# Performance work log

Hardware: AMD Instinct MI355X
Metric: run time of the kernel (lower is better)

The kernel has to match this reference:

```python
import jax, jax.numpy as jnp
import numpy as np

NUM_INPUTS = 16
NUM_HIDDEN = 256
NUM_LAYERS = 4
B = 16384


def setup_inputs() -> dict:
    key = jax.random.key(0)
    ks = jax.random.split(key, 8)
    H, N, L = NUM_HIDDEN, NUM_INPUTS, NUM_LAYERS
    x0 = jax.random.normal(ks[0], (B, N), dtype=jnp.float32)
    # input layer: Linear(2 -> H)
    W_in = jax.random.normal(ks[1], (2, H), dtype=jnp.float32) * (1.0 / np.sqrt(2.0))
    b_in = jnp.zeros((H,), dtype=jnp.float32)
    # L-1 intermediate layers: Linear(2H -> H), stacked
    W_mid = jax.random.normal(ks[2], (L - 1, 2 * H, H), dtype=jnp.float32) * (1.0 / np.sqrt(2.0 * H))
    b_mid = jnp.zeros((L - 1, H), dtype=jnp.float32)
    # slater: Linear(H -> N) with xavier-normal weight, zero bias
    W_sl = jax.random.normal(ks[3], (H, N), dtype=jnp.float32) * np.sqrt(2.0 / (H + N))
    b_sl = jnp.zeros((N,), dtype=jnp.float32)
    width = jnp.full((1,), 0.1, dtype=jnp.float32)
    return {"x0": x0, "W_in": W_in, "b_in": b_in, "W_mid": W_mid,
            "b_mid": b_mid, "W_sl": W_sl, "b_sl": b_sl, "width": width}


def _forward(x0, W_in, b_in, W_mid, b_mid, W_sl, b_sl, width):
    N = x0.shape[1]
    # input equivariant layer: f = stack(h, mean(h)) -> [B, N, 2]
    g = jnp.broadcast_to(x0.mean(axis=1, keepdims=True), x0.shape)
    f = jnp.stack((x0, g), axis=2)                       # [B, N, 2]
    h = jnp.tanh(jnp.einsum('bnf,fh->bnh', f, W_in) + b_in)  # [B, N, H]
    # intermediate equivariant layers with residual
    for i in range(W_mid.shape[0]):
        gm = jnp.broadcast_to(h.mean(axis=1, keepdims=True), h.shape)
        fm = jnp.concatenate((h, gm), axis=2)            # [B, N, 2H]
        h = jnp.tanh(jnp.einsum('bnf,fh->bnh', fm, W_mid[i]) + b_mid[i]) + h
    # slog slater determinant
    slater = jnp.einsum('bnh,hm->bnm', h, W_sl) + b_sl   # [B, N, N]
    sign, logabsdet = jnp.linalg.slogdet(slater)
    log_factorial = jnp.log(jnp.arange(1, N + 1, dtype=jnp.float32)).sum()
    log_bcs = -width[0] * jnp.sum(x0 ** 2, axis=1)       # [B]
    return sign, logabsdet - 0.5 * log_factorial + log_bcs


def reference(x0, W_in, b_in, W_mid, b_mid, W_sl, b_sl, width):
    return _forward(x0, W_in, b_in, W_mid, b_mid, W_sl, b_sl, width)
```

## Files before the change

### kernel.cpp

```cpp
#include <hip/hip_runtime.h>

#define BTOT 16384
#define NI   16
#define HD   256
#define BB   4
#define NMID 3
#define ASH  264
#define SLS  20
#define HALF_LOGFACT 15.3359295387f

typedef short  bf16x8 __attribute__((ext_vector_type(8)));
typedef float  f32x4  __attribute__((ext_vector_type(4)));

__device__ __forceinline__ unsigned short f2bf(float f) {
    unsigned u = __builtin_bit_cast(unsigned, f);
    u += 0x7FFFu + ((u >> 16) & 1u);
    return (unsigned short)(u >> 16);
}
__device__ __forceinline__ unsigned cvt_pk_bf16(float lo, float hi) {
    unsigned d;
    asm("v_cvt_pk_bf16_f32 %0, %1, %2" : "=v"(d) : "v"(lo), "v"(hi));
    return d;
}
__device__ __forceinline__ float bflo(unsigned u) { return __builtin_bit_cast(float, u << 16); }
__device__ __forceinline__ float bfhi(unsigned u) { return __builtin_bit_cast(float, u & 0xFFFF0000u); }
__device__ __forceinline__ float bcast(float x, int lane) {
    return __builtin_bit_cast(float,
        __builtin_amdgcn_readlane(__builtin_bit_cast(int, x), lane));
}
__device__ __forceinline__ float tanh5(float x) {
    float z = __builtin_amdgcn_exp2f(x * 2.885390081777927f);
    return __builtin_fmaf(-2.0f, __builtin_amdgcn_rcpf(1.0f + z), 1.0f);
}
#define LGKM_BAR() do { asm volatile("s_waitcnt lgkmcnt(0)" ::: "memory"); \
    __builtin_amdgcn_s_barrier(); __builtin_amdgcn_sched_barrier(0); } while (0)
#define LGKM_WAIT() do { asm volatile("s_waitcnt lgkmcnt(0)" ::: "memory"); \
    __builtin_amdgcn_sched_barrier(0); } while (0)

__global__ void prep_w(const float* __restrict__ Wmid, const float* __restrict__ Wsl,
                       unsigned short* __restrict__ wtc) {
    const int b = blockIdx.x;
    const int t = threadIdx.x;
    unsigned short* dst = wtc + (size_t)b * 8192;
    if (b < 48) {
        const int layer = b >> 4, ch = b & 15;
        const float* src = Wmid + (size_t)layer * (2 * HD * HD);
#pragma unroll 4
        for (int v = 0; v < 32; ++v) {
            int o = t * 32 + v;
            int kk = o & 7, j = (o >> 3) & 15, kg = o >> 7;
            dst[o] = f2bf(src[(8 * kg + kk) * HD + ch * 16 + j]);
        }
    } else {
#pragma unroll 4
        for (int v = 0; v < 32; ++v) {
            int o = t * 32 + v;
            int kk = o & 7, j = (o >> 3) & 15, kg = o >> 7;
            dst[o] = (kg < 32) ? f2bf(Wsl[(8 * kg + kk) * NI + j]) : (unsigned short)0;
        }
    }
}

struct __align__(16) SMem {
    union {
        unsigned short h[BB * NI * ASH];
        float slf[BB][NI * ASH / 2];
    } u;
    unsigned short stash[2 * NI * ASH];
    unsigned short gmgv[BB * HD];
};
static_assert(sizeof(SMem) == 52736, "R6-proven 3-blocks/CU size");

__global__ __launch_bounds__(256, 3)
void eqslater_mfma(const float* __restrict__ x0g,
                   const float* __restrict__ Win,
                   const float* __restrict__ bin,
                   const float* __restrict__ bmid,
                   const float* __restrict__ bsl,
                   const float* __restrict__ width,
                   const unsigned short* __restrict__ wtc,
                   float* __restrict__ out) {
    __shared__ SMem sm;
    const int tid = threadIdx.x;
    const int bbase = blockIdx.x * BB;
    const int w = tid >> 6;
    const int l = tid & 63;
    const int c = l & 15;
    const int g = l >> 4;
    const int j4 = 4 * g;
    const int B0 = 64 * w;

    const unsigned short* wlane = wtc + (size_t)g * 128 + (size_t)c * 8;

    float x0v = x0g[bbase * NI + l];
    {
        float ssum = x0v;
#pragma unroll
        for (int off = 8; off > 0; off >>= 1) ssum += __shfl_xor(ssum, off);
        const float gme = ssum * 0.0625f;
        const int jc = B0 + l;
        const float w0 = Win[jc], w1 = Win[HD + jc], bj = bin[jc];
#pragma unroll
        for (int el = 0; el < 4; ++el) {
            float ge = bcast(gme, el * 16);
            float gl = __builtin_fmaf(ge, w1, bj);
#pragma unroll 4
            for (int r = 0; r < NI; ++r) {
                float xv = bcast(x0v, el * 16 + r);
                float f = tanh5(__builtin_fmaf(xv, w0, gl));
                sm.u.h[(el * NI + r) * ASH + jc] =
                    (unsigned short)cvt_pk_bf16(f, f);
            }
        }
    }
    LGKM_BAR();

    bf16x8 afE[2][8], sbufG[8];

#pragma unroll 1
    for (int layer = 0; layer < NMID; ++layer) {
        {
            const int r32 = tid >> 3;
            const int seg = tid & 7;
            const unsigned short* srcp = &sm.u.h[(32 + r32) * ASH + seg * 32];
            unsigned short* dstp = &sm.stash[r32 * ASH + seg * 32];
#pragma unroll
            for (int p = 0; p < 4; ++p)
                *(uint4*)(dstp + p * 8) = *(const uint4*)(srcp + p * 8);
        }
        {
            const int el2 = l >> 4;
            const int c0 = B0 + (l & 15) * 4;
            float s0 = 0, s1 = 0, s2 = 0, s3 = 0;
#pragma unroll
            for (int r = 0; r < NI; ++r) {
                uint2 d = *(const uint2*)&sm.u.h[(el2 * NI + r) * ASH + c0];
                s0 += bflo(d.x); s1 += bfhi(d.x);
                s2 += bflo(d.y); s3 += bfhi(d.y);
            }
            uint2 go;
            go.x = cvt_pk_bf16(s0 * 0.0625f, s1 * 0.0625f);
            go.y = cvt_pk_bf16(s2 * 0.0625f, s3 * 0.0625f);
            *(uint2*)&sm.gmgv[el2 * HD + c0] = go;
        }
        LGKM_BAR();

#pragma unroll
        for (int s = 0; s < 8; ++s)
            sbufG[s] = *(const bf16x8*)&sm.gmgv[(c & 3) * HD + 32 * s + 8 * g];
        LGKM_BAR();

        const float* bml = bmid + layer * HD;

#pragma unroll 1
        for (int cc = 0; cc < 4; ++cc) {
            const int ch = 4 * w + cc;
            const unsigned short* cb2 = wlane + (size_t)(layer * 16 + ch) * 8192 + 4096;
            f32x4 accG = {0.f, 0.f, 0.f, 0.f};
#pragma unroll
            for (int half = 0; half < 2; ++half) {
                bf16x8 wfh[4];
#pragma unroll
                for (int s = 0; s < 4; ++s)
                    wfh[s] = *(const bf16x8*)(cb2 + (4 * half + s) * 512);
#pragma unroll
                for (int s = 0; s < 4; ++s)
                    accG = __builtin_amdgcn_mfma_f32_16x16x32_bf16(wfh[s], sbufG[4 * half + s], accG, 0, 0, 0);
            }
            const float4 bv = *(const float4*)&bml[ch * 16 + j4];
            if (c < 4) {
                uint2 go;
                go.x = cvt_pk_bf16(accG[0] + bv.x, accG[1] + bv.y);
                go.y = cvt_pk_bf16(accG[2] + bv.z, accG[3] + bv.w);
                *(uint2*)&sm.gmgv[c * HD + ch * 16 + j4] = go;
            }
        }

#pragma unroll
        for (int el = 0; el < 2; ++el)
#pragma unroll
            for (int s = 0; s < 8; ++s)
                afE[el][s] = *(const bf16x8*)&sm.u.h[(el * NI + c) * ASH + 32 * s + 8 * g];
        LGKM_BAR();

#pragma unroll 1
        for (int cc = 0; cc < 4; ++cc) {
            const int ch = 4 * w + cc;
            const unsigned short* cb = wlane + (size_t)(layer * 16 + ch) * 8192;
            f32x4 acc0 = {0.f,0.f,0.f,0.f}, acc1 = {0.f,0.f,0.f,0.f};
            f32x4 acc2 = {0.f,0.f,0.f,0.f}, acc3 = {0.f,0.f,0.f,0.f};
#pragma unroll
            for (int half = 0; half < 2; ++half) {
                bf16x8 wfh[4], sb[4];
#pragma unroll
                for (int s = 0; s < 4; ++s)
                    wfh[s] = *(const bf16x8*)(cb + (4 * half + s) * 512);
#pragma unroll
                for (int s = 0; s < 4; ++s) {
                    acc0 = __builtin_amdgcn_mfma_f32_16x16x32_bf16(wfh[s], afE[0][4 * half + s], acc0, 0, 0, 0);
                    acc1 = __builtin_amdgcn_mfma_f32_16x16x32_bf16(wfh[s], afE[1][4 * half + s], acc1, 0, 0, 0);
                }
#pragma unroll
                for (int s = 0; s < 4; ++s)
                    sb[s] = *(const bf16x8*)&sm.stash[c * ASH + 32 * (4 * half + s) + 8 * g];
#pragma unroll
                for (int s = 0; s < 4; ++s)
                    acc2 = __builtin_amdgcn_mfma_f32_16x16x32_bf16(wfh[s], sb[s], acc2, 0, 0, 0);
#pragma unroll
                for (int s = 0; s < 4; ++s)
                    sb[s] = *(const bf16x8*)&sm.stash[(NI + c) * ASH + 32 * (4 * half + s) + 8 * g];
#pragma unroll
                for (int s = 0; s < 4; ++s)
                    acc3 = __builtin_amdgcn_mfma_f32_16x16x32_bf16(wfh[s], sb[s], acc3, 0, 0, 0);
            }
#pragma unroll
            for (int el = 0; el < 4; ++el) {
                f32x4 acc = (el == 0) ? acc0 : (el == 1) ? acc1 : (el == 2) ? acc2 : acc3;
                const uint2 gd = *(const uint2*)&sm.gmgv[el * HD + ch * 16 + j4];
                unsigned short* hrow = &sm.u.h[(el * NI + c) * ASH + ch * 16 + j4];
                uint2 hd2 = *(const uint2*)hrow;
                float f0 = tanh5(acc[0] + bflo(gd.x)) + bflo(hd2.x);
                float f1 = tanh5(acc[1] + bfhi(gd.x)) + bfhi(hd2.x);
                float f2 = tanh5(acc[2] + bflo(gd.y)) + bflo(hd2.y);
                float f3 = tanh5(acc[3] + bfhi(gd.y)) + bfhi(hd2.y);
                uint2 wo; wo.x = cvt_pk_bf16(f0, f1); wo.y = cvt_pk_bf16(f2, f3);
                *(uint2*)hrow = wo;
            }
        }
        LGKM_BAR();
    }

    {
        const int e = w;
        bf16x8 sb8[8];
#pragma unroll
        for (int s = 0; s < 8; ++s)
            sb8[s] = *(const bf16x8*)&sm.u.h[(e * NI + c) * ASH + 32 * s + 8 * g];
        const unsigned short* cb = wlane + (size_t)48 * 8192;
        f32x4 a0 = {0.f,0.f,0.f,0.f}, a1 = {0.f,0.f,0.f,0.f};
#pragma unroll
        for (int s = 0; s < 4; ++s) {
            bf16x8 b0 = *(const bf16x8*)(cb + (2 * s) * 512);
            bf16x8 b1 = *(const bf16x8*)(cb + (2 * s + 1) * 512);
            a0 = __builtin_amdgcn_mfma_f32_16x16x32_bf16(b0, sb8[2 * s],     a0, 0, 0, 0);
            a1 = __builtin_amdgcn_mfma_f32_16x16x32_bf16(b1, sb8[2 * s + 1], a1, 0, 0, 0);
        }
        f32x4 sv = a0 + a1;
        const float4 bsv = *(const float4*)&bsl[j4];
        float* slp = &sm.u.slf[e][0];
        float4 o;
        o.x = sv[0] + bsv.x; o.y = sv[1] + bsv.y;
        o.z = sv[2] + bsv.z; o.w = sv[3] + bsv.w;
        *(float4*)&slp[c * SLS + j4] = o;
    }
    LGKM_WAIT();

    {
        const int e = w;
        const float* slp = &sm.u.slf[e][0];
        const int i = c;
        float M[16];
#pragma unroll
        for (int jj = 0; jj < 4; ++jj) {
            float4 vv = *(const float4*)&slp[i * SLS + 4 * jj];
            M[4 * jj] = vv.x; M[4 * jj + 1] = vv.y; M[4 * jj + 2] = vv.z; M[4 * jj + 3] = vv.w;
        }

        int elim = 0;
        unsigned chosen = 0;
        int invcnt = 0;
        float dsign = 1.f, logabs = 0.f;
#pragma unroll
        for (int k = 0; k < 16; ++k) {
            float myv = elim ? -1.f : __builtin_fabsf(M[k]);
            float maxv = myv;
#pragma unroll
            for (int off = 8; off > 0; off >>= 1)
                maxv = fmaxf(maxv, __shfl_xor(maxv, off));
            unsigned long long bal = __ballot(myv == maxv);
            const int p = (__ffsll((long long)bal) - 1) & 15;

            invcnt += __popc(chosen >> (p + 1));
            chosen |= 1u << p;
            if (i == p) elim = 1;

            float piv = bcast(M[k], p);
            float ap = fmaxf(__builtin_fabsf(piv), 1e-35f);
            logabs += __logf(ap);
            if (piv < 0.f) dsign = -dsign;
            float spiv = __builtin_copysignf(ap, piv);
            float mi = __fdividef(M[k], spiv);
#pragma unroll
            for (int j = k + 1; j < 16; ++j) {
                float pr = bcast(M[j], p);
                if (!elim) M[j] = __builtin_fmaf(-mi, pr, M[j]);
            }
        }
        if (invcnt & 1) dsign = -dsign;

        float xv = (l < NI) ? x0g[(bbase + w) * NI + l] : 0.f;
        float sq = xv * xv;
#pragma unroll
        for (int off = 8; off > 0; off >>= 1) sq += __shfl_xor(sq, off);

        if (l == 0) {
            out[bbase + w] = dsign;
            out[BTOT + bbase + w] = logabs - HALF_LOGFACT - width[0] * sq;
        }
    }
}

extern "C" void kernel_launch(void* const* d_in, const int* in_sizes, int n_in,
                              void* d_out, int out_size, void* d_ws, size_t ws_size,
                              hipStream_t stream) {
    const float* x0   = (const float*)d_in[0];
    const float* Win  = (const float*)d_in[1];
    const float* bin  = (const float*)d_in[2];
    const float* Wmid = (const float*)d_in[3];
    const float* bmid = (const float*)d_in[4];
    const float* Wsl  = (const float*)d_in[5];
    const float* bsl  = (const float*)d_in[6];
    const float* wid  = (const float*)d_in[7];
    float* out = (float*)d_out;

    unsigned short* wtc = (unsigned short*)d_ws;

    hipLaunchKernelGGL(prep_w, dim3(49), dim3(256), 0, stream, Wmid, Wsl, wtc);
    hipLaunchKernelGGL(eqslater_mfma, dim3(BTOT / BB), dim3(256), 0, stream,
                       x0, Win, bin, bmid, bsl, wid, wtc, out);
}
```

Before: 249.0 us.

## Prefetch next-chunk weights and split gm accumulator chain in mid layers

Moves the afE LDS loads to before the first barrier, so they overlap the gm-projection MFMAs. It also splits the gm-projection accumulator into two independent MFMA chains to shorten dependency latency. The main GEMM loop is software-pipelined: the first-half weights of the next chunk are loaded from global memory while the current chunk's second half computes. The trade-off is higher register pressure, and the full barrier becomes an LGKM wait, which depends on correct ordering of the gmgv writes and reads.

New measurement: 253.5 us. About the same (+1.8%).

```diff
diff --git a/kernel.cpp b/kernel.cpp
--- a/kernel.cpp
+++ b/kernel.cpp
@@ -148,6 +148,11 @@
 #pragma unroll
         for (int s = 0; s < 8; ++s)
             sbufG[s] = *(const bf16x8*)&sm.gmgv[(c & 3) * HD + 32 * s + 8 * g];
+#pragma unroll
+        for (int el = 0; el < 2; ++el)
+#pragma unroll
+            for (int s = 0; s < 8; ++s)
+                afE[el][s] = *(const bf16x8*)&sm.u.h[(el * NI + c) * ASH + 32 * s + 8 * g];
         LGKM_BAR();
 
         const float* bml = bmid + layer * HD;
@@ -156,17 +161,19 @@
         for (int cc = 0; cc < 4; ++cc) {
             const int ch = 4 * w + cc;
             const unsigned short* cb2 = wlane + (size_t)(layer * 16 + ch) * 8192 + 4096;
-            f32x4 accG = {0.f, 0.f, 0.f, 0.f};
+            f32x4 aG0 = {0.f,0.f,0.f,0.f}, aG1 = {0.f,0.f,0.f,0.f};
 #pragma unroll
             for (int half = 0; half < 2; ++half) {
                 bf16x8 wfh[4];
 #pragma unroll
                 for (int s = 0; s < 4; ++s)
                     wfh[s] = *(const bf16x8*)(cb2 + (4 * half + s) * 512);
-#pragma unroll
-                for (int s = 0; s < 4; ++s)
-                    accG = __builtin_amdgcn_mfma_f32_16x16x32_bf16(wfh[s], sbufG[4 * half + s], accG, 0, 0, 0);
-            }
+                aG0 = __builtin_amdgcn_mfma_f32_16x16x32_bf16(wfh[0], sbufG[4 * half],     aG0, 0, 0, 0);
+                aG1 = __builtin_amdgcn_mfma_f32_16x16x32_bf16(wfh[1], sbufG[4 * half + 1], aG1, 0, 0, 0);
+                aG0 = __builtin_amdgcn_mfma_f32_16x16x32_bf16(wfh[2], sbufG[4 * half + 2], aG0, 0, 0, 0);
+                aG1 = __builtin_amdgcn_mfma_f32_16x16x32_bf16(wfh[3], sbufG[4 * half + 3], aG1, 0, 0, 0);
+            }
+            f32x4 accG = aG0 + aG1;
             const float4 bv = *(const float4*)&bml[ch * 16 + j4];
             if (c < 4) {
                 uint2 go;
@@ -175,44 +182,66 @@
                 *(uint2*)&sm.gmgv[c * HD + ch * 16 + j4] = go;
             }
         }
-
-#pragma unroll
-        for (int el = 0; el < 2; ++el)
-#pragma unroll
-            for (int s = 0; s < 8; ++s)
-                afE[el][s] = *(const bf16x8*)&sm.u.h[(el * NI + c) * ASH + 32 * s + 8 * g];
-        LGKM_BAR();
-
+        LGKM_WAIT();
+
+        bf16x8 wfA[4];
+        {
+            const unsigned short* cb0 = wlane + (size_t)(layer * 16 + 4 * w) * 8192;
+#pragma unroll
+            for (int s = 0; s < 4; ++s)
+                wfA[s] = *(const bf16x8*)(cb0 + s * 512);
+        }
 #pragma unroll 1
         for (int cc = 0; cc < 4; ++cc) {
             const int ch = 4 * w + cc;
             const unsigned short* cb = wlane + (size_t)(layer * 16 + ch) * 8192;
+            bf16x8 wfB[4], sb[4];
+#pragma unroll
+            for (int s = 0; s < 4; ++s)
+                wfB[s] = *(const bf16x8*)(cb + (4 + s) * 512);
+
             f32x4 acc0 = {0.f,0.f,0.f,0.f}, acc1 = {0.f,0.f,0.f,0.f};
             f32x4 acc2 = {0.f,0.f,0.f,0.f}, acc3 = {0.f,0.f,0.f,0.f};
 #pragma unroll
-            for (int half = 0; half < 2; ++half) {
-                bf16x8 wfh[4], sb[4];
+            for (int s = 0; s < 4; ++s) {
+                acc0 = __builtin_amdgcn_mfma_f32_16x16x32_bf16(wfA[s], afE[0][s], acc0, 0, 0, 0);
+                acc1 = __builtin_amdgcn_mfma_f32_16x16x32_bf16(wfA[s], afE[1][s], acc1, 0, 0, 0);
+            }
+#pragma unroll
+            for (int s = 0; s < 4; ++s)
+                sb[s] = *(const bf16x8*)&sm.stash[c * ASH + 32 * s + 8 * g];
+#pragma unroll
+            for (int s = 0; s < 4; ++s)
+                acc2 = __builtin_amdgcn_mfma_f32_16x16x32_bf16(wfA[s], sb[s], acc2, 0, 0, 0);
+#pragma unroll
+            for (int s = 0; s < 4; ++s)
+                sb[s] = *(const bf16x8*)&sm.stash[(NI + c) * ASH + 32 * s + 8 * g];
+#pragma unroll
+            for (int s = 0; s < 4; ++s)
+                acc3 = __builtin_amdgcn_mfma_f32_16x16x32_bf16(wfA[s], sb[s], acc3, 0, 0, 0);
+            if (cc < 3) {
 #pragma unroll
                 for (int s = 0; s < 4; ++s)
-                    wfh[s] = *(const bf16x8*)(cb + (4 * half + s) * 512);
-#pragma unroll
-                for (int s = 0; s < 4; ++s) {
-                    acc0 = __builtin_amdgcn_mfma_f32_16x16x32_bf16(wfh[s], afE[0][4 * half + s], acc0, 0, 0, 0);
-                    acc1 = __builtin_amdgcn_mfma_f32_16x16x32_bf16(wfh[s], afE[1][4 * half + s], acc1, 0, 0, 0);
-                }
-#pragma unroll
-                for (int s = 0; s < 4; ++s)
-                    sb[s] = *(const bf16x8*)&sm.stash[c * ASH + 32 * (4 * half + s) + 8 * g];
-#pragma unroll
-                for (int s = 0; s < 4; ++s)
-                    acc2 = __builtin_amdgcn_mfma_f32_16x16x32_bf16(wfh[s], sb[s], acc2, 0, 0, 0);
-#pragma unroll
-                for (int s = 0; s < 4; ++s)
-                    sb[s] = *(const bf16x8*)&sm.stash[(NI + c) * ASH + 32 * (4 * half + s) + 8 * g];
-#pragma unroll
-                for (int s = 0; s < 4; ++s)
-                    acc3 = __builtin_amdgcn_mfma_f32_16x16x32_bf16(wfh[s], sb[s], acc3, 0, 0, 0);
-            }
+                    wfA[s] = *(const bf16x8*)(cb + 8192 + s * 512);
+            }
+#pragma unroll
+            for (int s = 0; s < 4; ++s) {
+                acc0 = __builtin_amdgcn_mfma_f32_16x16x32_bf16(wfB[s], afE[0][4 + s], acc0, 0, 0, 0);
+                acc1 = __builtin_amdgcn_mfma_f32_16x16x32_bf16(wfB[s], afE[1][4 + s], acc1, 0, 0, 0);
+            }
+#pragma unroll
+            for (int s = 0; s < 4; ++s)
+                sb[s] = *(const bf16x8*)&sm.stash[c * ASH + 32 * (4 + s) + 8 * g];
+#pragma unroll
+            for (int s = 0; s < 4; ++s)
+                acc2 = __builtin_amdgcn_mfma_f32_16x16x32_bf16(wfB[s], sb[s], acc2, 0, 0, 0);
+#pragma unroll
+            for (int s = 0; s < 4; ++s)
+                sb[s] = *(const bf16x8*)&sm.stash[(NI + c) * ASH + 32 * (4 + s) + 8 * g];
+#pragma unroll
+            for (int s = 0; s < 4; ++s)
+                acc3 = __builtin_amdgcn_mfma_f32_16x16x32_bf16(wfB[s], sb[s], acc3, 0, 0, 0);
+
 #pragma unroll
             for (int el = 0; el < 4; ++el) {
                 f32x4 acc = (el == 0) ? acc0 : (el == 1) ? acc1 : (el == 2) ? acc2 : acc3;
```

## Halve batch elements per block to drop stash buffer and raise occupancy

Applied to the files above, without the earlier changes.

Each block now processes 2 batch elements instead of 4. This removes the shared-memory stash copy and the extra accumulators, shrinks LDS so four blocks fit per CU, and doubles the grid. The tradeoff is that every weight fragment loaded from global/L2 is reused by only two MFMA streams instead of four, so weight traffic per element doubles. Also, half the waves sit idle during the slater and determinant stage.

Measured after the change: 299.0 us. 20.1% more time.

```diff
diff --git a/kernel.cpp b/kernel.cpp
--- a/kernel.cpp
+++ b/kernel.cpp
@@ -3,7 +3,7 @@
 #define BTOT 16384
 #define NI   16
 #define HD   256
-#define BB   4
+#define BB   2
 #define NMID 3
 #define ASH  264
 #define SLS  20
@@ -66,12 +66,11 @@
         unsigned short h[BB * NI * ASH];
         float slf[BB][NI * ASH / 2];
     } u;
-    unsigned short stash[2 * NI * ASH];
     unsigned short gmgv[BB * HD];
 };
-static_assert(sizeof(SMem) == 52736, "R6-proven 3-blocks/CU size");
-
-__global__ __launch_bounds__(256, 3)
+static_assert(sizeof(SMem) == 17920, "4 blocks/CU needs <= ~40KB");
+
+__global__ __launch_bounds__(256, 4)
 void eqslater_mfma(const float* __restrict__ x0g,
                    const float* __restrict__ Win,
                    const float* __restrict__ bin,
@@ -92,17 +91,16 @@
 
     const unsigned short* wlane = wtc + (size_t)g * 128 + (size_t)c * 8;
 
-    float x0v = x0g[bbase * NI + l];
+    float x0v = x0g[bbase * NI + (l & 31)];
     {
         float ssum = x0v;
 #pragma unroll
         for (int off = 8; off > 0; off >>= 1) ssum += __shfl_xor(ssum, off);
-        const float gme = ssum * 0.0625f;
         const int jc = B0 + l;
         const float w0 = Win[jc], w1 = Win[HD + jc], bj = bin[jc];
 #pragma unroll
-        for (int el = 0; el < 4; ++el) {
-            float ge = bcast(gme, el * 16);
+        for (int el = 0; el < BB; ++el) {
+            float ge = bcast(ssum, el * 16) * 0.0625f;
             float gl = __builtin_fmaf(ge, w1, bj);
 #pragma unroll 4
             for (int r = 0; r < NI; ++r) {
@@ -115,39 +113,26 @@
     }
     LGKM_BAR();
 
-    bf16x8 afE[2][8], sbufG[8];
+    bf16x8 afE[BB][8], sbufG[8];
 
 #pragma unroll 1
     for (int layer = 0; layer < NMID; ++layer) {
         {
-            const int r32 = tid >> 3;
-            const int seg = tid & 7;
-            const unsigned short* srcp = &sm.u.h[(32 + r32) * ASH + seg * 32];
-            unsigned short* dstp = &sm.stash[r32 * ASH + seg * 32];
-#pragma unroll
-            for (int p = 0; p < 4; ++p)
-                *(uint4*)(dstp + p * 8) = *(const uint4*)(srcp + p * 8);
-        }
-        {
-            const int el2 = l >> 4;
-            const int c0 = B0 + (l & 15) * 4;
-            float s0 = 0, s1 = 0, s2 = 0, s3 = 0;
+            const int el2 = l >> 5;
+            const int c0 = B0 + (l & 31) * 2;
+            float s0 = 0, s1 = 0;
 #pragma unroll
             for (int r = 0; r < NI; ++r) {
-                uint2 d = *(const uint2*)&sm.u.h[(el2 * NI + r) * ASH + c0];
-                s0 += bflo(d.x); s1 += bfhi(d.x);
-                s2 += bflo(d.y); s3 += bfhi(d.y);
-            }
-            uint2 go;
-            go.x = cvt_pk_bf16(s0 * 0.0625f, s1 * 0.0625f);
-            go.y = cvt_pk_bf16(s2 * 0.0625f, s3 * 0.0625f);
-            *(uint2*)&sm.gmgv[el2 * HD + c0] = go;
+                unsigned d = *(const unsigned*)&sm.u.h[(el2 * NI + r) * ASH + c0];
+                s0 += bflo(d); s1 += bfhi(d);
+            }
+            *(unsigned*)&sm.gmgv[el2 * HD + c0] = cvt_pk_bf16(s0 * 0.0625f, s1 * 0.0625f);
         }
         LGKM_BAR();
 
 #pragma unroll
         for (int s = 0; s < 8; ++s)
-            sbufG[s] = *(const bf16x8*)&sm.gmgv[(c & 3) * HD + 32 * s + 8 * g];
+            sbufG[s] = *(const bf16x8*)&sm.gmgv[(c & 1) * HD + 32 * s + 8 * g];
         LGKM_BAR();
 
         const float* bml = bmid + layer * HD;
@@ -156,19 +141,21 @@
         for (int cc = 0; cc < 4; ++cc) {
             const int ch = 4 * w + cc;
             const unsigned short* cb2 = wlane + (size_t)(layer * 16 + ch) * 8192 + 4096;
-            f32x4 accG = {0.f, 0.f, 0.f, 0.f};
+            f32x4 aG0 = {0.f,0.f,0.f,0.f}, aG1 = {0.f,0.f,0.f,0.f};
 #pragma unroll
             for (int half = 0; half < 2; ++half) {
                 bf16x8 wfh[4];
 #pragma unroll
                 for (int s = 0; s < 4; ++s)
                     wfh[s] = *(const bf16x8*)(cb2 + (4 * half + s) * 512);
-#pragma unroll
-                for (int s = 0; s < 4; ++s)
-                    accG = __builtin_amdgcn_mfma_f32_16x16x32_bf16(wfh[s], sbufG[4 * half + s], accG, 0, 0, 0);
-            }
+                aG0 = __builtin_amdgcn_mfma_f32_16x16x32_bf16(wfh[0], sbufG[4 * half],     aG0, 0, 0, 0);
+                aG1 = __builtin_amdgcn_mfma_f32_16x16x32_bf16(wfh[1], sbufG[4 * half + 1], aG1, 0, 0, 0);
+                aG0 = __builtin_amdgcn_mfma_f32_16x16x32_bf16(wfh[2], sbufG[4 * half + 2], aG0, 0, 0, 0);
+                aG1 = __builtin_amdgcn_mfma_f32_16x16x32_bf16(wfh[3], sbufG[4 * half + 3], aG1, 0, 0, 0);
+            }
+            f32x4 accG = aG0 + aG1;
             const float4 bv = *(const float4*)&bml[ch * 16 + j4];
-            if (c < 4) {
+            if (c < BB) {
                 uint2 go;
                 go.x = cvt_pk_bf16(accG[0] + bv.x, accG[1] + bv.y);
                 go.y = cvt_pk_bf16(accG[2] + bv.z, accG[3] + bv.w);
@@ -177,7 +164,7 @@
         }
 
 #pragma unroll
-        for (int el = 0; el < 2; ++el)
+        for (int el = 0; el < BB; ++el)
 #pragma unroll
             for (int s = 0; s < 8; ++s)
                 afE[el][s] = *(const bf16x8*)&sm.u.h[(el * NI + c) * ASH + 32 * s + 8 * g];
@@ -188,10 +175,9 @@
             const int ch = 4 * w + cc;
             const unsigned short* cb = wlane + (size_t)(layer * 16 + ch) * 8192;
             f32x4 acc0 = {0.f,0.f,0.f,0.f}, acc1 = {0.f,0.f,0.f,0.f};
-            f32x4 acc2 = {0.f,0.f,0.f,0.f}, acc3 = {0.f,0.f,0.f,0.f};
 #pragma unroll
             for (int half = 0; half < 2; ++half) {
-                bf16x8 wfh[4], sb[4];
+                bf16x8 wfh[4];
 #pragma unroll
                 for (int s = 0; s < 4; ++s)
                     wfh[s] = *(const bf16x8*)(cb + (4 * half + s) * 512);
@@ -200,22 +186,10 @@
                     acc0 = __builtin_amdgcn_mfma_f32_16x16x32_bf16(wfh[s], afE[0][4 * half + s], acc0, 0, 0, 0);
                     acc1 = __builtin_amdgcn_mfma_f32_16x16x32_bf16(wfh[s], afE[1][4 * half + s], acc1, 0, 0, 0);
                 }
-#pragma unroll
-                for (int s = 0; s < 4; ++s)
-                    sb[s] = *(const bf16x8*)&sm.stash[c * ASH + 32 * (4 * half + s) + 8 * g];
-#pragma unroll
-                for (int s = 0; s < 4; ++s)
-                    acc2 = __builtin_amdgcn_mfma_f32_16x16x32_bf16(wfh[s], sb[s], acc2, 0, 0, 0);
-#pragma unroll
-                for (int s = 0; s < 4; ++s)
-                    sb[s] = *(const bf16x8*)&sm.stash[(NI + c) * ASH + 32 * (4 * half + s) + 8 * g];
-#pragma unroll
-                for (int s = 0; s < 4; ++s)
-                    acc3 = __builtin_amdgcn_mfma_f32_16x16x32_bf16(wfh[s], sb[s], acc3, 0, 0, 0);
-            }
-#pragma unroll
-            for (int el = 0; el < 4; ++el) {
-                f32x4 acc = (el == 0) ? acc0 : (el == 1) ? acc1 : (el == 2) ? acc2 : acc3;
+            }
+#pragma unroll
+            for (int el = 0; el < BB; ++el) {
+                f32x4 acc = (el == 0) ? acc0 : acc1;
                 const uint2 gd = *(const uint2*)&sm.gmgv[el * HD + ch * 16 + j4];
                 unsigned short* hrow = &sm.u.h[(el * NI + c) * ASH + ch * 16 + j4];
                 uint2 hd2 = *(const uint2*)hrow;
@@ -230,33 +204,32 @@
         LGKM_BAR();
     }
 
-    {
+    if (w < BB) {
         const int e = w;
-        bf16x8 sb8[8];
-#pragma unroll
-        for (int s = 0; s < 8; ++s)
-            sb8[s] = *(const bf16x8*)&sm.u.h[(e * NI + c) * ASH + 32 * s + 8 * g];
-        const unsigned short* cb = wlane + (size_t)48 * 8192;
-        f32x4 a0 = {0.f,0.f,0.f,0.f}, a1 = {0.f,0.f,0.f,0.f};
-#pragma unroll
-        for (int s = 0; s < 4; ++s) {
-            bf16x8 b0 = *(const bf16x8*)(cb + (2 * s) * 512);
-            bf16x8 b1 = *(const bf16x8*)(cb + (2 * s + 1) * 512);
-            a0 = __builtin_amdgcn_mfma_f32_16x16x32_bf16(b0, sb8[2 * s],     a0, 0, 0, 0);
-            a1 = __builtin_amdgcn_mfma_f32_16x16x32_bf16(b1, sb8[2 * s + 1], a1, 0, 0, 0);
-        }
-        f32x4 sv = a0 + a1;
-        const float4 bsv = *(const float4*)&bsl[j4];
-        float* slp = &sm.u.slf[e][0];
-        float4 o;
-        o.x = sv[0] + bsv.x; o.y = sv[1] + bsv.y;
-        o.z = sv[2] + bsv.z; o.w = sv[3] + bsv.w;
-        *(float4*)&slp[c * SLS + j4] = o;
-    }
-    LGKM_WAIT();
-
-    {
-        const int e = w;
+        {
+            bf16x8 sb8[8];
+#pragma unroll
+            for (int s = 0; s < 8; ++s)
+                sb8[s] = *(const bf16x8*)&sm.u.h[(e * NI + c) * ASH + 32 * s + 8 * g];
+            const unsigned short* cb = wlane + (size_t)48 * 8192;
+            f32x4 a0 = {0.f,0.f,0.f,0.f}, a1 = {0.f,0.f,0.f,0.f};
+#pragma unroll
+            for (int s = 0; s < 4; ++s) {
+                bf16x8 b0 = *(const bf16x8*)(cb + (2 * s) * 512);
+                bf16x8 b1 = *(const bf16x8*)(cb + (2 * s + 1) * 512);
+                a0 = __builtin_amdgcn_mfma_f32_16x16x32_bf16(b0, sb8[2 * s],     a0, 0, 0, 0);
+                a1 = __builtin_amdgcn_mfma_f32_16x16x32_bf16(b1, sb8[2 * s + 1], a1, 0, 0, 0);
+            }
+            f32x4 sv = a0 + a1;
+            const float4 bsv = *(const float4*)&bsl[j4];
+            float* slp = &sm.u.slf[e][0];
+            float4 o;
+            o.x = sv[0] + bsv.x; o.y = sv[1] + bsv.y;
+            o.z = sv[2] + bsv.z; o.w = sv[3] + bsv.w;
+            *(float4*)&slp[c * SLS + j4] = o;
+        }
+        LGKM_WAIT();
+
         const float* slp = &sm.u.slf[e][0];
         const int i = c;
         float M[16];
@@ -298,14 +271,14 @@
         }
         if (invcnt & 1) dsign = -dsign;
 
-        float xv = (l < NI) ? x0g[(bbase + w) * NI + l] : 0.f;
+        float xv = (l < NI) ? x0g[(bbase + e) * NI + l] : 0.f;
         float sq = xv * xv;
 #pragma unroll
         for (int off = 8; off > 0; off >>= 1) sq += __shfl_xor(sq, off);
 
         if (l == 0) {
-            out[bbase + w] = dsign;
-            out[BTOT + bbase + w] = logabs - HALF_LOGFACT - width[0] * sq;
+            out[bbase + e] = dsign;
+            out[BTOT + bbase + e] = logabs - HALF_LOGFACT - width[0] * sq;
         }
     }
 }
```
